# Kernel tuning notes

Measured on AMD Instinct MI355X. Metric: run time of the kernel, lower is better.

## Reference

```python
import jax, jax.numpy as jnp
import numpy as np

N = 100000
E = 3200000
IN_DIM, HID, RED, EMB = 2, 64, 32, 32
LN_EPS = 1e-5


def gcn_conv(x, W, b, row, col, w_full, dinv):
    # x:[N,F_in] W:[F_in,F_out]; PyG GCNConv: lin (no bias) -> normalized scatter-add -> + bias
    xw = x @ W                                  # [N,F_out]
    norm = dinv[row] * w_full * dinv[col]       # [E+N]
    msgs = norm[:, None] * xw[row]              # gather from source nodes
    out = jax.ops.segment_sum(msgs, col, num_segments=N)
    return out + b


def layer_norm(x, g, b):
    mu = jnp.mean(x, axis=-1, keepdims=True)
    var = jnp.mean((x - mu) ** 2, axis=-1, keepdims=True)
    return (x - mu) * jax.lax.rsqrt(var + LN_EPS) * g + b


def setup_inputs() -> dict:
    key = jax.random.key(0)
    ks = jax.random.split(key, 12)
    def glorot(k, shape):
        lim = float(np.sqrt(6.0 / (shape[0] + shape[1])))
        return jax.random.uniform(k, shape, jnp.float32, -lim, lim)
    return {
        "x": jax.random.normal(ks[0], (N, IN_DIM), jnp.float32),
        "edge_weight": jax.random.uniform(ks[1], (E,), jnp.float32),
        "W1": glorot(ks[2], (IN_DIM, HID)), "b1": jnp.zeros((HID,), jnp.float32),
        "rW1": glorot(ks[3], (IN_DIM, HID)), "rb1": jnp.zeros((HID,), jnp.float32),
        "g1": jnp.ones((HID,), jnp.float32), "be1": jnp.zeros((HID,), jnp.float32),
        "W2": glorot(ks[4], (HID, RED)), "b2": jnp.zeros((RED,), jnp.float32),
        "rW2": glorot(ks[5], (HID, RED)), "rb2": jnp.zeros((RED,), jnp.float32),
        "g2": jnp.ones((RED,), jnp.float32), "be2": jnp.zeros((RED,), jnp.float32),
        "fcW": glorot(ks[6], (RED, 1)), "fcb": jnp.zeros((1,), jnp.float32),
        "pW": glorot(ks[7], (RED, EMB)), "pb": jnp.zeros((EMB,), jnp.float32),
        "edge_index": jax.random.randint(ks[8], (2, E), 0, N, jnp.int64)
        if jax.config.read("jax_enable_x64") else jax.random.randint(ks[8], (2, E), 0, N, jnp.int32),
    }


def reference(x, edge_weight, W1, b1, rW1, rb1, g1, be1, W2, b2, rW2, rb2, g2, be2,
              fcW, fcb, pW, pb, edge_index):
    row, col = edge_index[0], edge_index[1]
    # add self-loops with weight 1 (PyG gcn_norm default)
    loops = jnp.arange(N, dtype=row.dtype)
    row_f = jnp.concatenate([row, loops])
    col_f = jnp.concatenate([col, loops])
    w_f = jnp.concatenate([edge_weight, jnp.ones((N,), edge_weight.dtype)])
    deg = jax.ops.segment_sum(w_f, col_f, num_segments=N)
    dinv = jnp.where(deg > 0, jax.lax.rsqrt(jnp.where(deg > 0, deg, 1.0)), 0.0)

    x1 = gcn_conv(x, W1, b1, row_f, col_f, w_f, dinv) + (x @ rW1 + rb1)
    x1 = jax.nn.relu(layer_norm(x1, g1, be1))
    x2 = gcn_conv(x1, W2, b2, row_f, col_f, w_f, dinv) + (x1 @ rW2 + rb2)
    x2 = jax.nn.relu(layer_norm(x2, g2, be2))

    logits = (x2 @ fcW + fcb)[:, 0]
    proj = x2 @ pW + pb
    nrm = jnp.linalg.norm(proj, axis=1, keepdims=True)
    emb = proj / jnp.maximum(nrm, 1e-12)
    return logits, emb
```

## Files before the change

kernel.cpp:

```cpp
#include <hip/hip_runtime.h>
#include <hip/hip_bf16.h>

#define NN 100000
#define NE 3200000
#define LN_EPS 1e-5f
#define NBUCK 196
#define TILE 4096
#define NTILE 782
#define CAP 20480
#define L1NB 16

__global__ void k_ginit(int* __restrict__ gcur) {
    int b = threadIdx.x;
    if (b < NBUCK) gcur[b] = b * CAP;
}

__global__ __launch_bounds__(256) void k_partA(
        const int* __restrict__ row, const int* __restrict__ col,
        const float* __restrict__ w, int* __restrict__ gcur,
        int2* __restrict__ tmp) {
    __shared__ int2 sbuf[TILE];
    __shared__ int  gpos[TILE];
    __shared__ int  lhist[NBUCK];
    __shared__ int  lofs[NBUCK];
    __shared__ int  lbase[NBUCK];
    __shared__ int  wsum[4];
    int t = threadIdx.x;
    long base_e = (long)blockIdx.x * TILE;
    int nt = NE - base_e < TILE ? (int)(NE - base_e) : TILE;

    for (int b = t; b < NBUCK; b += 256) lhist[b] = 0;
    __syncthreads();

    int pk[16]; float wv16[16]; int bri[16];
    #pragma unroll
    for (int i = 0; i < 16; ++i) {
        int j = t + i * 256;
        if (j < nt) {
            int e = (int)base_e + j;
            int r = row[e], c = col[e];
            pk[i] = r | ((c & 511) << 17);
            wv16[i] = w[e];
            int b = c >> 9;
            int rk = atomicAdd(&lhist[b], 1);
            bri[i] = (b << 16) | rk;
        } else bri[i] = -1;
    }
    __syncthreads();

    {
        int v = (t < NBUCK) ? lhist[t] : 0;
        int lane = t & 63;
        int inc = v;
        #pragma unroll
        for (int off = 1; off < 64; off <<= 1) {
            int u = __shfl_up(inc, off, 64);
            if (lane >= off) inc += u;
        }
        if (lane == 63) wsum[t >> 6] = inc;
        __syncthreads();
        int wv = t >> 6;
        int woff = 0;
        for (int j = 0; j < 4; ++j) if (j < wv) woff += wsum[j];
        if (t < NBUCK) {
            lofs[t] = woff + inc - v;
            lbase[t] = atomicAdd(&gcur[t], v);
        }
    }
    __syncthreads();

    #pragma unroll
    for (int i = 0; i < 16; ++i) {
        if (bri[i] >= 0) {
            int b = bri[i] >> 16, rk = bri[i] & 0xFFFF;
            int slot = lofs[b] + rk;
            sbuf[slot] = make_int2(pk[i], __float_as_int(wv16[i]));
            gpos[slot] = lbase[b] + rk;
        }
    }
    __syncthreads();

    #pragma unroll
    for (int i = 0; i < 16; ++i) {
        int j = t + i * 256;
        if (j < nt) tmp[gpos[j]] = sbuf[j];
    }
}

__global__ void k_cscan(const int* __restrict__ gcur, int* __restrict__ obase,
                        int* __restrict__ ptr) {
    __shared__ int sm[256];
    int t = threadIdx.x;
    int v = (t < NBUCK) ? (gcur[t] - t * CAP) : 0;
    sm[t] = v;
    __syncthreads();
    for (int off = 1; off < 256; off <<= 1) {
        int u = (t >= off) ? sm[t - off] : 0;
        __syncthreads();
        sm[t] += u;
        __syncthreads();
    }
    if (t < NBUCK) obase[t] = sm[t] - v;
    if (t == 0) ptr[NN] = NE;
}

__global__ __launch_bounds__(512) void k_partB(
        const int* __restrict__ gcur, const int* __restrict__ obase,
        const int2* __restrict__ tmp, const float* __restrict__ x,
        unsigned* __restrict__ csrp, int* __restrict__ ptr,
        float* __restrict__ dinv, float2* __restrict__ y) {
    __shared__ int   nh[512];
    __shared__ float wsumf[512];
    __shared__ int   wscan[8];
    int b = blockIdx.x;
    int t = threadIdx.x;
    int start = b * CAP, end = gcur[b];
    int outb = obase[b];
    nh[t] = 0; wsumf[t] = 0.0f;
    __syncthreads();
    for (int j = start + t; j < end; j += 512) {
        int2 rec = tmp[j];
        int cl = ((unsigned)rec.x) >> 17;
        atomicAdd(&nh[cl], 1);
        atomicAdd(&wsumf[cl], __int_as_float(rec.y));
    }
    __syncthreads();
    int v = nh[t];
    int lane = t & 63;
    int inc = v;
    #pragma unroll
    for (int off = 1; off < 64; off <<= 1) {
        int u = __shfl_up(inc, off, 64);
        if (lane >= off) inc += u;
    }
    if (lane == 63) wscan[t >> 6] = inc;
    __syncthreads();
    int wv = t >> 6;
    int woff = 0;
    #pragma unroll
    for (int j = 0; j < 8; ++j) if (j < wv) woff += wscan[j];
    int ex = outb + woff + inc - v;
    int gn = b * 512 + t;
    if (gn < NN) {
        ptr[gn] = ex;
        float di = rsqrtf(wsumf[t] + 1.0f);
        dinv[gn] = di;
        float2 xv = *(const float2*)(x + 2 * gn);
        y[gn] = make_float2(di * xv.x, di * xv.y);
    }
    __syncthreads();
    nh[t] = ex;
    __syncthreads();
    for (int j = start + t; j < end; j += 512) {
        int2 rec = tmp[j];
        int cl = ((unsigned)rec.x) >> 17;
        int r = rec.x & 0x1FFFF;
        float wf = __int_as_float(rec.y);
        __hip_bfloat16 hb = __float2bfloat16(wf);
        unsigned short wbits = *reinterpret_cast<unsigned short*>(&hb);
        int pos = atomicAdd(&nh[cl], 1);
        csrp[pos] = ((unsigned)r << 15) | (unsigned)wbits;
    }
}

__global__ void k_agg1(const int* __restrict__ ptr, const unsigned* __restrict__ csrp,
                       const float* __restrict__ dinv, const float2* __restrict__ y,
                       float* __restrict__ agg1) {
    int t = blockIdx.x * blockDim.x + threadIdx.x;
    int node = t >> 5, lane = t & 31;
    if (node >= NN) return;
    int start = ptr[node], n = ptr[node + 1] - start;
    float a0 = 0.0f, a1 = 0.0f;
    for (int j = lane; j < n; j += 32) {
        unsigned p = __builtin_nontemporal_load(csrp + start + j);
        int r = p >> 15;
        float wf = __uint_as_float((p & 0x7FFFu) << 16);
        float2 yv = y[r];
        a0 += wf * yv.x;
        a1 += wf * yv.y;
    }
    #pragma unroll
    for (int m = 16; m >= 1; m >>= 1) {
        a0 += __shfl_xor(a0, m, 32);
        a1 += __shfl_xor(a1, m, 32);
    }
    if (lane == 0) {
        float di = dinv[node];
        float2 yv = y[node];
        agg1[2 * node]     = di * (a0 + yv.x);
        agg1[2 * node + 1] = di * (a1 + yv.y);
    }
}

__global__ __launch_bounds__(256) void k_l1t2(
        const float* __restrict__ agg1, const float* __restrict__ x,
        const float* __restrict__ dinv,
        const float* __restrict__ W1, const float* __restrict__ b1,
        const float* __restrict__ rW1, const float* __restrict__ rb1,
        const float* __restrict__ g1, const float* __restrict__ be1,
        const float* __restrict__ W2, const float* __restrict__ b2,
        const float* __restrict__ rW2, const float* __restrict__ rb2,
        __hip_bfloat16* __restrict__ t2, float* __restrict__ agg2i) {
    __shared__ float wT[64][68];
    __shared__ float xs[L1NB][68];
    int tid = threadIdx.x;
    for (int i = tid; i < 4096; i += 256) {
        int j = i >> 6, o = i & 63;
        wT[o][j] = (o < 32) ? W2[j * 32 + o] : rW2[j * 32 + (o - 32)];
    }
    int wid = tid >> 6, lane = tid & 63;
    int base = blockIdx.x * L1NB;
    float w10 = W1[lane], w11 = W1[64 + lane];
    float r10 = rW1[lane], r11 = rW1[64 + lane];
    float bb = b1[lane] + rb1[lane];
    float gg = g1[lane], be = be1[lane];
    #pragma unroll
    for (int sub = 0; sub < 4; ++sub) {
        int n = base + wid * 4 + sub;
        float a0 = agg1[2 * n], a1 = agg1[2 * n + 1];
        float xa = x[2 * n], xb = x[2 * n + 1];
        float v = a0 * w10 + a1 * w11 + xa * r10 + xb * r11 + bb;
        float s = v;
        #pragma unroll
        for (int m = 32; m >= 1; m >>= 1) s += __shfl_xor(s, m, 64);
        float mean = s * (1.0f / 64.0f);
        float e = v - mean;
        float s2 = e * e;
        #pragma unroll
        for (int m = 32; m >= 1; m >>= 1) s2 += __shfl_xor(s2, m, 64);
        float var = s2 * (1.0f / 64.0f);
        xs[wid * 4 + sub][lane] = fmaxf(e * rsqrtf(var + LN_EPS) * gg + be, 0.0f);
    }
    __syncthreads();
    int o = lane, g = wid;
    const float4* wrow = (const float4*)&wT[o][0];
    const float4* x0 = (const float4*)&xs[g][0];
    const float4* x1r = (const float4*)&xs[g + 4][0];
    const float4* x2r = (const float4*)&xs[g + 8][0];
    const float4* x3r = (const float4*)&xs[g + 12][0];
    float acc0 = 0.0f, acc1 = 0.0f, acc2 = 0.0f, acc3 = 0.0f;
    #pragma unroll
    for (int jq = 0; jq < 16; ++jq) {
        float4 wv = wrow[jq];
        float4 a = x0[jq], b = x1r[jq], c = x2r[jq], d = x3r[jq];
        acc0 += wv.x * a.x + wv.y * a.y + wv.z * a.z + wv.w * a.w;
        acc1 += wv.x * b.x + wv.y * b.y + wv.z * b.z + wv.w * b.w;
        acc2 += wv.x * c.x + wv.y * c.y + wv.z * c.z + wv.w * c.w;
        acc3 += wv.x * d.x + wv.y * d.y + wv.z * d.z + wv.w * d.w;
    }
    float res0 = __shfl_xor(acc0, 32, 64);
    float res1 = __shfl_xor(acc1, 32, 64);
    float res2 = __shfl_xor(acc2, 32, 64);
    float res3 = __shfl_xor(acc3, 32, 64);
    if (o < 32) {
        float accs[4] = {acc0, acc1, acc2, acc3};
        float ress[4] = {res0, res1, res2, res3};
        #pragma unroll
        for (int i = 0; i < 4; ++i) {
            int n = base + g + 4 * i;
            float di = dinv[n];
            t2[n * 32 + o] = __float2bfloat16(accs[i] * di);
            agg2i[n * 32 + o] = accs[i] * di * di + b2[o] + ress[i] + rb2[o];
        }
    }
}

__global__ __launch_bounds__(256) void k_agg2fin(
        const int* __restrict__ ptr, const unsigned* __restrict__ csrp,
        const float* __restrict__ dinv, const __hip_bfloat16* __restrict__ t2,
        const float* __restrict__ agg2i,
        const float* __restrict__ g2, const float* __restrict__ be2,
        const float* __restrict__ fcW, const float* __restrict__ fcb,
        const float* __restrict__ pW, const float* __restrict__ pb,
        float* __restrict__ out) {
    int node = (blockIdx.x * blockDim.x + threadIdx.x) >> 5;
    int k = threadIdx.x & 31;
    if (node >= NN) return;
    int start = ptr[node], n = ptr[node + 1] - start;
    float acc = 0.0f;
    int j4 = n & ~3;
    for (int j = 0; j < j4; j += 4) {
        uint4 pp = *(const uint4*)(csrp + start + j);
        {
            float wf = __uint_as_float((pp.x & 0x7FFFu) << 16);
            acc += wf * __bfloat162float(t2[(pp.x >> 15) * 32 + k]);
        }
        {
            float wf = __uint_as_float((pp.y & 0x7FFFu) << 16);
            acc += wf * __bfloat162float(t2[(pp.y >> 15) * 32 + k]);
        }
        {
            float wf = __uint_as_float((pp.z & 0x7FFFu) << 16);
            acc += wf * __bfloat162float(t2[(pp.z >> 15) * 32 + k]);
        }
        {
            float wf = __uint_as_float((pp.w & 0x7FFFu) << 16);
            acc += wf * __bfloat162float(t2[(pp.w >> 15) * 32 + k]);
        }
    }
    for (int j = j4; j < n; ++j) {
        unsigned p = csrp[start + j];
        float wf = __uint_as_float((p & 0x7FFFu) << 16);
        acc += wf * __bfloat162float(t2[(p >> 15) * 32 + k]);
    }
    float di = dinv[node];
    float v = agg2i[node * 32 + k] + di * acc;
    float s = v;
    #pragma unroll
    for (int m = 16; m >= 1; m >>= 1) s += __shfl_xor(s, m, 32);
    float mean = s * (1.0f / 32.0f);
    float e = v - mean;
    float s2 = e * e;
    #pragma unroll
    for (int m = 16; m >= 1; m >>= 1) s2 += __shfl_xor(s2, m, 32);
    float var = s2 * (1.0f / 32.0f);
    float x2 = fmaxf(e * rsqrtf(var + LN_EPS) * g2[k] + be2[k], 0.0f);
    float lg = x2 * fcW[k];
    #pragma unroll
    for (int m = 16; m >= 1; m >>= 1) lg += __shfl_xor(lg, m, 32);
    if (k == 0) out[node] = lg + fcb[0];
    float acc2 = pb[k];
    #pragma unroll
    for (int j = 0; j < 32; ++j) {
        float xj = __shfl(x2, j, 32);
        acc2 += xj * pW[j * 32 + k];
    }
    float n2 = acc2 * acc2;
    #pragma unroll
    for (int m = 16; m >= 1; m >>= 1) n2 += __shfl_xor(n2, m, 32);
    float nrm = sqrtf(n2);
    out[NN + node * 32 + k] = acc2 / fmaxf(nrm, 1e-12f);
}

extern "C" void kernel_launch(void* const* d_in, const int* in_sizes, int n_in,
                              void* d_out, int out_size, void* d_ws, size_t ws_size,
                              hipStream_t stream) {
    const float* x   = (const float*)d_in[0];
    const float* ew  = (const float*)d_in[1];
    const float* W1  = (const float*)d_in[2];
    const float* b1  = (const float*)d_in[3];
    const float* rW1 = (const float*)d_in[4];
    const float* rb1 = (const float*)d_in[5];
    const float* g1  = (const float*)d_in[6];
    const float* be1 = (const float*)d_in[7];
    const float* W2  = (const float*)d_in[8];
    const float* b2  = (const float*)d_in[9];
    const float* rW2 = (const float*)d_in[10];
    const float* rb2 = (const float*)d_in[11];
    const float* g2  = (const float*)d_in[12];
    const float* be2 = (const float*)d_in[13];
    const float* fcW = (const float*)d_in[14];
    const float* fcb = (const float*)d_in[15];
    const float* pW  = (const float*)d_in[16];
    const float* pb  = (const float*)d_in[17];
    const int*   ei  = (const int*)d_in[18];
    const int* row = ei;
    const int* col = ei + NE;

    char* p = (char*)d_ws;
    unsigned* csrp = (unsigned*)p;            p += (size_t)NE * 4;
    char* regionA = p;                        p += (size_t)NBUCK * CAP * 8;
    __hip_bfloat16* t2 = (__hip_bfloat16*)regionA;
    float* agg2i = (float*)(regionA + (size_t)NN * 32 * 2);
    int2*  tmp   = (int2*)regionA;
    float* dinv  = (float*)p;                 p += (size_t)NN * 4;
    float2* y    = (float2*)p;                p += (size_t)NN * 8;
    float* agg1  = (float*)p;                 p += (size_t)2 * NN * 4;
    int*   ptr   = (int*)p;                   p += (size_t)(NN + 1) * 4;
    int*   gcur  = (int*)p;                   p += 256 * 4;
    int*   obase = (int*)p;                   p += 256 * 4;

    float* out = (float*)d_out;
    const int TB = 256;
    const int NODE32 = (NN * 32 + TB - 1) / TB;

    k_ginit<<<1, 256, 0, stream>>>(gcur);
    k_partA<<<NTILE, 256, 0, stream>>>(row, col, ew, gcur, tmp);
    k_cscan<<<1, 256, 0, stream>>>(gcur, obase, ptr);
    k_partB<<<NBUCK, 512, 0, stream>>>(gcur, obase, tmp, x, csrp, ptr, dinv, y);
    k_agg1<<<NODE32, TB, 0, stream>>>(ptr, csrp, dinv, y, agg1);
    k_l1t2<<<NN / L1NB, 256, 0, stream>>>(agg1, x, dinv, W1, b1, rW1, rb1, g1, be1,
                                          W2, b2, rW2, rb2, t2, agg2i);
    k_agg2fin<<<NODE32, TB, 0, stream>>>(ptr, csrp, dinv, t2, agg2i,
                                         g2, be2, fcW, fcb, pW, pb, out);
}
```

Baseline: 235.7 us.

## Fuse layer-1 aggregation into CSR scatter pass, halve partition tile, unroll agg2 by 8

The bucket partition kernel is split in two. The second pass now accumulates the layer-1 two-feature aggregation in shared-memory atomics while it writes the CSR entries, which removes the separate k_agg1 kernel and its re-read of the CSR array. The partition tile size drops to 2048 edges, doubling the block count in partA. The layer-2 gather loop is unrolled to 8 neighbours with independent loads to raise memory-level parallelism. The trade-offs are a second launch over the temp buffer, plus contention on the shared float atomics and a change in summation order.

```diff
diff --git a/kernel.cpp b/kernel.cpp
--- a/kernel.cpp
+++ b/kernel.cpp
@@ -5,8 +5,8 @@
 #define NE 3200000
 #define LN_EPS 1e-5f
 #define NBUCK 196
-#define TILE 4096
-#define NTILE 782
+#define TILE 2048
+#define NTILE 1563
 #define CAP 20480
 #define L1NB 16
 
@@ -32,9 +32,9 @@
     for (int b = t; b < NBUCK; b += 256) lhist[b] = 0;
     __syncthreads();
 
-    int pk[16]; float wv16[16]; int bri[16];
-    #pragma unroll
-    for (int i = 0; i < 16; ++i) {
+    int pk[8]; float wv16[8]; int bri[8];
+    #pragma unroll
+    for (int i = 0; i < 8; ++i) {
         int j = t + i * 256;
         if (j < nt) {
             int e = (int)base_e + j;
@@ -70,7 +70,7 @@
     __syncthreads();
 
     #pragma unroll
-    for (int i = 0; i < 16; ++i) {
+    for (int i = 0; i < 8; ++i) {
         if (bri[i] >= 0) {
             int b = bri[i] >> 16, rk = bri[i] & 0xFFFF;
             int slot = lofs[b] + rk;
@@ -81,7 +81,7 @@
     __syncthreads();
 
     #pragma unroll
-    for (int i = 0; i < 16; ++i) {
+    for (int i = 0; i < 8; ++i) {
         int j = t + i * 256;
         if (j < nt) tmp[gpos[j]] = sbuf[j];
     }
@@ -104,11 +104,10 @@
     if (t == 0) ptr[NN] = NE;
 }
 
-__global__ __launch_bounds__(512) void k_partB(
+__global__ __launch_bounds__(512) void k_partB1(
         const int* __restrict__ gcur, const int* __restrict__ obase,
         const int2* __restrict__ tmp, const float* __restrict__ x,
-        unsigned* __restrict__ csrp, int* __restrict__ ptr,
-        float* __restrict__ dinv, float2* __restrict__ y) {
+        int* __restrict__ ptr, float* __restrict__ dinv, float2* __restrict__ y) {
     __shared__ int   nh[512];
     __shared__ float wsumf[512];
     __shared__ int   wscan[8];
@@ -148,8 +147,22 @@
         float2 xv = *(const float2*)(x + 2 * gn);
         y[gn] = make_float2(di * xv.x, di * xv.y);
     }
-    __syncthreads();
-    nh[t] = ex;
+}
+
+__global__ __launch_bounds__(512) void k_partB2(
+        const int* __restrict__ gcur, const int2* __restrict__ tmp,
+        const int* __restrict__ ptr, const float* __restrict__ dinv,
+        const float2* __restrict__ y,
+        unsigned* __restrict__ csrp, float* __restrict__ agg1) {
+    __shared__ int   nh[512];
+    __shared__ float a0s[512];
+    __shared__ float a1s[512];
+    int b = blockIdx.x;
+    int t = threadIdx.x;
+    int start = b * CAP, end = gcur[b];
+    int gn = b * 512 + t;
+    nh[t] = (gn < NN) ? ptr[gn] : 0;
+    a0s[t] = 0.0f; a1s[t] = 0.0f;
     __syncthreads();
     for (int j = start + t; j < end; j += 512) {
         int2 rec = tmp[j];
@@ -160,35 +173,16 @@
         unsigned short wbits = *reinterpret_cast<unsigned short*>(&hb);
         int pos = atomicAdd(&nh[cl], 1);
         csrp[pos] = ((unsigned)r << 15) | (unsigned)wbits;
-    }
-}
-
-__global__ void k_agg1(const int* __restrict__ ptr, const unsigned* __restrict__ csrp,
-                       const float* __restrict__ dinv, const float2* __restrict__ y,
-                       float* __restrict__ agg1) {
-    int t = blockIdx.x * blockDim.x + threadIdx.x;
-    int node = t >> 5, lane = t & 31;
-    if (node >= NN) return;
-    int start = ptr[node], n = ptr[node + 1] - start;
-    float a0 = 0.0f, a1 = 0.0f;
-    for (int j = lane; j < n; j += 32) {
-        unsigned p = __builtin_nontemporal_load(csrp + start + j);
-        int r = p >> 15;
-        float wf = __uint_as_float((p & 0x7FFFu) << 16);
         float2 yv = y[r];
-        a0 += wf * yv.x;
-        a1 += wf * yv.y;
-    }
-    #pragma unroll
-    for (int m = 16; m >= 1; m >>= 1) {
-        a0 += __shfl_xor(a0, m, 32);
-        a1 += __shfl_xor(a1, m, 32);
-    }
-    if (lane == 0) {
-        float di = dinv[node];
-        float2 yv = y[node];
-        agg1[2 * node]     = di * (a0 + yv.x);
-        agg1[2 * node + 1] = di * (a1 + yv.y);
+        atomicAdd(&a0s[cl], wf * yv.x);
+        atomicAdd(&a1s[cl], wf * yv.y);
+    }
+    __syncthreads();
+    if (gn < NN) {
+        float di = dinv[gn];
+        float2 yv = y[gn];
+        agg1[2 * gn]     = di * (a0s[t] + yv.x);
+        agg1[2 * gn + 1] = di * (a1s[t] + yv.y);
     }
 }
 
@@ -278,27 +272,30 @@
     if (node >= NN) return;
     int start = ptr[node], n = ptr[node + 1] - start;
     float acc = 0.0f;
-    int j4 = n & ~3;
-    for (int j = 0; j < j4; j += 4) {
-        uint4 pp = *(const uint4*)(csrp + start + j);
-        {
-            float wf = __uint_as_float((pp.x & 0x7FFFu) << 16);
-            acc += wf * __bfloat162float(t2[(pp.x >> 15) * 32 + k]);
-        }
-        {
-            float wf = __uint_as_float((pp.y & 0x7FFFu) << 16);
-            acc += wf * __bfloat162float(t2[(pp.y >> 15) * 32 + k]);
-        }
-        {
-            float wf = __uint_as_float((pp.z & 0x7FFFu) << 16);
-            acc += wf * __bfloat162float(t2[(pp.z >> 15) * 32 + k]);
-        }
-        {
-            float wf = __uint_as_float((pp.w & 0x7FFFu) << 16);
-            acc += wf * __bfloat162float(t2[(pp.w >> 15) * 32 + k]);
-        }
-    }
-    for (int j = j4; j < n; ++j) {
+    int j8 = n & ~7;
+    for (int j = 0; j < j8; j += 8) {
+        uint4 pa = *(const uint4*)(csrp + start + j);
+        uint4 pb4 = *(const uint4*)(csrp + start + j + 4);
+        float wf0 = __uint_as_float((pa.x & 0x7FFFu) << 16);
+        float wf1 = __uint_as_float((pa.y & 0x7FFFu) << 16);
+        float wf2 = __uint_as_float((pa.z & 0x7FFFu) << 16);
+        float wf3 = __uint_as_float((pa.w & 0x7FFFu) << 16);
+        float wf4 = __uint_as_float((pb4.x & 0x7FFFu) << 16);
+        float wf5 = __uint_as_float((pb4.y & 0x7FFFu) << 16);
+        float wf6 = __uint_as_float((pb4.z & 0x7FFFu) << 16);
+        float wf7 = __uint_as_float((pb4.w & 0x7FFFu) << 16);
+        float v0 = __bfloat162float(t2[(pa.x >> 15) * 32 + k]);
+        float v1 = __bfloat162float(t2[(pa.y >> 15) * 32 + k]);
+        float v2 = __bfloat162float(t2[(pa.z >> 15) * 32 + k]);
+        float v3 = __bfloat162float(t2[(pa.w >> 15) * 32 + k]);
+        float v4 = __bfloat162float(t2[(pb4.x >> 15) * 32 + k]);
+        float v5 = __bfloat162float(t2[(pb4.y >> 15) * 32 + k]);
+        float v6 = __bfloat162float(t2[(pb4.z >> 15) * 32 + k]);
+        float v7 = __bfloat162float(t2[(pb4.w >> 15) * 32 + k]);
+        acc += wf0 * v0 + wf1 * v1 + wf2 * v2 + wf3 * v3
+             + wf4 * v4 + wf5 * v5 + wf6 * v6 + wf7 * v7;
+    }
+    for (int j = j8; j < n; ++j) {
         unsigned p = csrp[start + j];
         float wf = __uint_as_float((p & 0x7FFFu) << 16);
         acc += wf * __bfloat162float(t2[(p >> 15) * 32 + k]);
@@ -377,8 +374,8 @@
     k_ginit<<<1, 256, 0, stream>>>(gcur);
     k_partA<<<NTILE, 256, 0, stream>>>(row, col, ew, gcur, tmp);
     k_cscan<<<1, 256, 0, stream>>>(gcur, obase, ptr);
-    k_partB<<<NBUCK, 512, 0, stream>>>(gcur, obase, tmp, x, csrp, ptr, dinv, y);
-    k_agg1<<<NODE32, TB, 0, stream>>>(ptr, csrp, dinv, y, agg1);
+    k_partB1<<<NBUCK, 512, 0, stream>>>(gcur, obase, tmp, x, ptr, dinv, y);
+    k_partB2<<<NBUCK, 512, 0, stream>>>(gcur, tmp, ptr, dinv, y, csrp, agg1);
     k_l1t2<<<NN / L1NB, 256, 0, stream>>>(agg1, x, dinv, W1, b1, rW1, rb1, g1, be1,
                                           W2, b2, rW2, rb2, t2, agg2i);
     k_agg2fin<<<NODE32, TB, 0, stream>>>(ptr, csrp, dinv, t2, agg2i,
```

New measurement: 240.0 us. About the same (+1.8%).
